# Performance work log

Hardware: AMD Instinct MI355X
Metric: run time of the kernel (lower is better)

Reference implementation:

```python
import jax, jax.numpy as jnp
import numpy as np

EPS = 1e-6
HEADS = 8
DIM_HEAD = 64
SCALE = 16.0
DIM = 1024
INNER = HEADS * DIM_HEAD


def _l2norm(t):
    return t / jnp.clip(jnp.linalg.norm(t, axis=-1, keepdims=True), 1e-12)


def setup_inputs() -> dict:
    key = jax.random.key(0)
    k1, k2, k3, k4 = jax.random.split(key, 4)
    b, n = 2, 4096
    x = jax.random.normal(k1, (b, n, DIM), dtype=jnp.float32)
    # weights stored as [in, out] so application is x @ W
    Wq = jax.random.normal(k2, (DIM, INNER), dtype=jnp.float32) * 0.02
    Wkv = jax.random.normal(k3, (DIM, 2 * INNER), dtype=jnp.float32) * 0.02
    Wo = jax.random.normal(k4, (INNER, DIM), dtype=jnp.float32) * 0.02
    return {"x": x, "Wq": Wq, "Wkv": Wkv, "Wo": Wo}


def reference(x, Wq, Wkv, Wo):
    b, n, _ = x.shape
    q = (x @ Wq).reshape(b, n, HEADS, DIM_HEAD).transpose(0, 2, 1, 3)  # b h n d
    kv = x @ Wkv
    k = kv[..., :INNER].reshape(b, n, HEADS, DIM_HEAD).transpose(0, 2, 1, 3)
    v = kv[..., INNER:].reshape(b, n, HEADS, DIM_HEAD).transpose(0, 2, 1, 3)
    q = _l2norm(q)
    k = _l2norm(k)
    # cosine-sim attention: logits = scale * (q.k) - scale, logits <= 0 so exp is stable
    logits = jnp.einsum('bhid,bhjd->bhij', q, k) * SCALE - SCALE
    p = jnp.exp(logits)
    row_sums = jnp.clip(p.sum(axis=-1, keepdims=True), EPS)  # matches per-block EPS clamp in dense case
    out = jnp.einsum('bhij,bhjd->bhid', p, v) / row_sums  # b h n d
    out = out.transpose(0, 2, 1, 3).reshape(b, n, INNER)
    return out @ Wo
```

## Files before the change

kernel.cpp:

```cpp
#include <hip/hip_runtime.h>


typedef _Float16 f16;
typedef _Float16 f16x4 __attribute__((ext_vector_type(4)));
typedef _Float16 f16x8 __attribute__((ext_vector_type(8)));
typedef float f32x4 __attribute__((ext_vector_type(4)));

#define MFMA_F16(a, b, c) __builtin_amdgcn_mfma_f32_16x16x32_f16((a), (b), (c), 0, 0, 0)

#define QSCALE 23.083120654223414f
#define EXPBIAS -9.083120654223414f

__device__ __forceinline__ void gl_lds16(const void* g, void* l) {
  __builtin_amdgcn_global_load_lds(
      (const __attribute__((address_space(1))) void*)g,
      (__attribute__((address_space(3))) void*)l, 16, 0, 0);
}

__global__ void convert_x_kernel(const float* __restrict__ x, f16* __restrict__ xh, int n8) {
  int i = blockIdx.x * 256 + threadIdx.x;
  if (i >= n8) return;
  const float4* xv = (const float4*)x;
  float4 a = xv[2 * i], b = xv[2 * i + 1];
  f16x8 o;
  o[0] = (f16)a.x; o[1] = (f16)a.y; o[2] = (f16)a.z; o[3] = (f16)a.w;
  o[4] = (f16)b.x; o[5] = (f16)b.y; o[6] = (f16)b.z; o[7] = (f16)b.w;
  ((f16x8*)xh)[i] = o;
}

__global__ void transpose_w_kernel(const float* __restrict__ W, int ldw, int col0,
                                   int K, f16* __restrict__ out) {
  __shared__ float t[64][65];
  int tx = threadIdx.x, ty = threadIdx.y;
  int c0 = blockIdx.x * 64, k0 = blockIdx.y * 64;
#pragma unroll
  for (int i = 0; i < 8; i++)
    t[ty + i * 8][tx] = W[(long)(k0 + ty + i * 8) * ldw + col0 + c0 + tx];
  __syncthreads();
#pragma unroll
  for (int i = 0; i < 8; i++)
    out[(long)(c0 + ty + i * 8) * K + k0 + tx] = (f16)t[tx][ty + i * 8];
}

__global__ void transpose_v_kernel(const f16* __restrict__ Vb, f16* __restrict__ Vt, int n) {
  __shared__ f16 t[64 * 64];
  const int tid = threadIdx.x;
  const int bh = blockIdx.y;
  const int n0 = blockIdx.x * 64;
  const f16* src = Vb + ((long)bh * n + n0) * 64;
  const int j = tid >> 3, c = tid & 7;
  f16x8 v0 = *(const f16x8*)(src + j * 64 + c * 8);
  f16x8 v1 = *(const f16x8*)(src + (j + 32) * 64 + c * 8);
  *(f16x8*)(&t[j * 64 + ((c ^ (j & 7)) << 3)]) = v0;
  *(f16x8*)(&t[(j + 32) * 64 + ((c ^ (j & 7)) << 3)]) = v1;
  __syncthreads();
  const int d = tid >> 3, cj = tid & 7;
  f16x8 o0, o1;
#pragma unroll
  for (int e = 0; e < 8; e++) {
    int jj = cj * 8 + e;
    o0[e] = t[jj * 64 + (((d >> 3) ^ (jj & 7)) << 3) + (d & 7)];
    o1[e] = t[jj * 64 + ((((d + 32) >> 3) ^ (jj & 7)) << 3) + ((d + 32) & 7)];
  }
  *(f16x8*)(Vt + ((long)bh * 64 + d) * n + n0 + cj * 8) = o0;
  *(f16x8*)(Vt + ((long)bh * 64 + d + 32) * n + n0 + cj * 8) = o1;
}

template <int MODE>
__global__ __launch_bounds__(256, 2)
void gemm_kernel(const f16* __restrict__ A, const f16* __restrict__ Bt,
                 float* __restrict__ C,
                 f16* __restrict__ Qb, f16* __restrict__ Kb, f16* __restrict__ Vb,
                 int M, int N, int K) {
  __shared__ f16 As[128 * 32];
  __shared__ f16 Bs[128 * 32];
  const int tid = threadIdx.x;
  const int lane = tid & 63;
  const int wid = tid >> 6;
  const int wr = wid >> 1, wc = wid & 1;
  const int lr = lane & 15, lk = lane >> 4;
  const int lin = blockIdx.x;
  const int bx = ((lin & 7) << 3) | ((lin >> 3) & 7);
  const int by = lin >> 6;
  const long m0 = (long)bx * 128;
  const int n0 = by * 128;

  f32x4 acc[4][4] = {};

  const int c0 = tid, c1 = tid + 256;
  const int ar0 = c0 >> 2, ah0 = (c0 & 3) ^ ((ar0 >> 1) & 3);
  const int ar1 = c1 >> 2, ah1 = (c1 & 3) ^ ((ar1 >> 1) & 3);
  const f16* pa0 = A + (m0 + ar0) * K + ah0 * 8;
  const f16* pa1 = A + (m0 + ar1) * K + ah1 * 8;
  const f16* pb0 = Bt + (long)(n0 + ar0) * K + ah0 * 8;
  const f16* pb1 = Bt + (long)(n0 + ar1) * K + ah1 * 8;

  for (int k0 = 0; k0 < K; k0 += 32) {
    __syncthreads();
    gl_lds16(pa0 + k0, As + c0 * 8);
    gl_lds16(pa1 + k0, As + c1 * 8);
    gl_lds16(pb0 + k0, Bs + c0 * 8);
    gl_lds16(pb1 + k0, Bs + c1 * 8);
    __syncthreads();

    f16x8 af[4], bf[4];
#pragma unroll
    for (int mi = 0; mi < 4; mi++) {
      int row = wr * 64 + mi * 16 + lr;
      int ch = lk ^ ((row >> 1) & 3);
      af[mi] = *(const f16x8*)(As + row * 32 + ch * 8);
    }
#pragma unroll
    for (int ni = 0; ni < 4; ni++) {
      int row = wc * 64 + ni * 16 + lr;
      int ch = lk ^ ((row >> 1) & 3);
      bf[ni] = *(const f16x8*)(Bs + row * 32 + ch * 8);
    }
    __builtin_amdgcn_s_setprio(1);
#pragma unroll
    for (int mi = 0; mi < 4; mi++)
#pragma unroll
      for (int ni = 0; ni < 4; ni++)
        acc[mi][ni] = MFMA_F16(af[mi], bf[ni], acc[mi][ni]);
    __builtin_amdgcn_s_setprio(0);
  }

  if (MODE == 0) {
#pragma unroll
    for (int mi = 0; mi < 4; mi++) {
      long mrow = m0 + wr * 64 + mi * 16 + lk * 4;
#pragma unroll
      for (int r = 0; r < 4; r++)
#pragma unroll
        for (int ni = 0; ni < 4; ni++)
          C[(mrow + r) * N + n0 + wc * 64 + ni * 16 + lr] = acc[mi][ni][r];
    }
  } else {
    const int region = by >> 2;
    const int head = (by & 3) * 2 + wc;
    f16* buf = (region == 0) ? Qb : ((region == 1) ? Kb : Vb);
    const float nscale = (region == 0) ? QSCALE : 1.f;
#pragma unroll
    for (int mi = 0; mi < 4; mi++) {
      float scl[4];
      if (region < 2) {
#pragma unroll
        for (int r = 0; r < 4; r++) {
          float s2 = 0.f;
#pragma unroll
          for (int ni = 0; ni < 4; ni++) s2 += acc[mi][ni][r] * acc[mi][ni][r];
          s2 += __shfl_xor(s2, 1);
          s2 += __shfl_xor(s2, 2);
          s2 += __shfl_xor(s2, 4);
          s2 += __shfl_xor(s2, 8);
          scl[r] = nscale / fmaxf(sqrtf(s2), 1e-12f);
        }
      } else {
#pragma unroll
        for (int r = 0; r < 4; r++) scl[r] = 1.f;
      }
#pragma unroll
      for (int r = 0; r < 4; r++) {
        int m = (int)m0 + wr * 64 + mi * 16 + lk * 4 + r;
        int bb = m >> 12, nn = m & 4095;
        f16* dst = buf + (((long)(bb * 8 + head) * 4096 + nn) << 6);
#pragma unroll
        for (int ni = 0; ni < 4; ni++)
          dst[ni * 16 + lr] = (f16)(acc[mi][ni][r] * scl[r]);
      }
    }
  }
}

__global__ __launch_bounds__(512, 4)
void attn_kernel(const f16* __restrict__ Qb, const f16* __restrict__ Kb,
                 const f16* __restrict__ Vt, f16* __restrict__ Ob, int n) {
  __shared__ f16 Ks[2][128 * 64];
  __shared__ f16 Vs[2][64 * 128];
  __shared__ f16 Ps[8][16 * 64];
  const int tid = threadIdx.x, lane = tid & 63, wid = tid >> 6;
  const int lr = lane & 15, lk = lane >> 4;
  const int lin = blockIdx.x;
  const int bh = (lin & 7) | ((lin >> 8) << 3);
  const int qx = (lin >> 3) & 31;
  const long nl = n;
  const f16* Qg = Qb + (long)bh * nl * 64;
  const f16* Kg = Kb + (long)bh * nl * 64;
  const f16* Vg = Vt + (long)bh * 64 * nl;
  const int q0 = qx * 128 + wid * 16;

  f16x8 qf[2];
#pragma unroll
  for (int kc = 0; kc < 2; kc++)
    qf[kc] = *(const f16x8*)(Qg + (long)(q0 + lr) * 64 + kc * 32 + lk * 8);

  const int krow = tid >> 3;
  const int kcol = ((tid & 7) ^ (krow & 7)) * 8;
  const int vrow = tid >> 4;
  const int vcol = ((tid & 15) ^ (vrow & 15)) * 8;

  f32x4 oacc[4] = {};
  f32x4 osum = {0.f, 0.f, 0.f, 0.f};
  const f32x4 initv = {EXPBIAS, EXPBIAS, EXPBIAS, EXPBIAS};
  f16x8 ones;
#pragma unroll
  for (int e = 0; e < 8; e++) ones[e] = (f16)1.f;

  gl_lds16(Kg + (long)krow * 64 + kcol, &Ks[0][tid * 8]);
  gl_lds16(Kg + (long)(krow + 64) * 64 + kcol, &Ks[0][tid * 8 + 4096]);
  gl_lds16(Vg + (long)vrow * nl + vcol, &Vs[0][tid * 8]);
  gl_lds16(Vg + (long)(vrow + 32) * nl + vcol, &Vs[0][tid * 8 + 4096]);
  __syncthreads();

  const int nt = n >> 7;
  for (int t = 0; t < nt; t++) {
    const int cur = t & 1;
    if (t + 1 < nt) {
      const long j0 = (long)(t + 1) << 7;
      gl_lds16(Kg + (j0 + krow) * 64 + kcol, &Ks[cur ^ 1][tid * 8]);
      gl_lds16(Kg + (j0 + krow + 64) * 64 + kcol, &Ks[cur ^ 1][tid * 8 + 4096]);
      gl_lds16(Vg + (long)vrow * nl + j0 + vcol, &Vs[cur ^ 1][tid * 8]);
      gl_lds16(Vg + (long)(vrow + 32) * nl + j0 + vcol, &Vs[cur ^ 1][tid * 8 + 4096]);
    }

    f32x4 s[8];
    __builtin_amdgcn_s_setprio(1);
#pragma unroll
    for (int jt = 0; jt < 8; jt++) {
      const int j = jt * 16 + lr;
      const f16x8 kf0 = *(const f16x8*)(&Ks[cur][j * 64 + ((lk ^ (j & 7)) << 3)]);
      const f16x8 kf1 = *(const f16x8*)(&Ks[cur][j * 64 + (((4 + lk) ^ (j & 7)) << 3)]);
      f32x4 acc0 = MFMA_F16(kf0, qf[0], initv);
      s[jt] = MFMA_F16(kf1, qf[1], acc0);
    }
    __builtin_amdgcn_s_setprio(0);

#pragma unroll
    for (int sub = 0; sub < 2; sub++) {
#pragma unroll
      for (int jt2 = 0; jt2 < 4; jt2++) {
        const f32x4 sv = s[sub * 4 + jt2];
        const float p0 = __builtin_amdgcn_exp2f(sv[0]);
        const float p1 = __builtin_amdgcn_exp2f(sv[1]);
        const float p2 = __builtin_amdgcn_exp2f(sv[2]);
        const float p3 = __builtin_amdgcn_exp2f(sv[3]);
        const auto h01 = __builtin_amdgcn_cvt_pkrtz(p0, p1);
        const auto h23 = __builtin_amdgcn_cvt_pkrtz(p2, p3);
        f16x4 pk;
        pk[0] = h01[0]; pk[1] = h01[1]; pk[2] = h23[0]; pk[3] = h23[1];
        const int c16 = jt2 * 2 + (lk >> 1);
        *(f16x4*)(&Ps[wid][lr * 64 + ((c16 ^ (lr & 7)) << 3) + ((lk & 1) << 2)]) = pk;
      }

      __builtin_amdgcn_s_setprio(1);
#pragma unroll
      for (int kc2 = 0; kc2 < 2; kc2++) {
        const int c16 = kc2 * 4 + lk;
        const f16x8 pa = *(const f16x8*)(&Ps[wid][lr * 64 + ((c16 ^ (lr & 7)) << 3)]);
        f16x8 vf[4];
#pragma unroll
        for (int dt = 0; dt < 4; dt++) {
          const int d = dt * 16 + lr;
          vf[dt] = *(const f16x8*)(&Vs[cur][d * 128 + (((sub * 8 + kc2 * 4 + lk) ^ (d & 15)) << 3)]);
        }
        osum = MFMA_F16(pa, ones, osum);
#pragma unroll
        for (int dt = 0; dt < 4; dt++)
          oacc[dt] = MFMA_F16(pa, vf[dt], oacc[dt]);
      }
      __builtin_amdgcn_s_setprio(0);
    }

    __syncthreads();
  }

  const int bb = bh >> 3, hh = bh & 7;
#pragma unroll
  for (int r = 0; r < 4; r++) {
    const float inv = 1.f / fmaxf(osum[r], 0.016384f);
    const int qq = q0 + lk * 4 + r;
    f16* dst = Ob + (((long)(bb * 4096 + qq)) << 9) + hh * 64;
#pragma unroll
    for (int dt = 0; dt < 4; dt++)
      dst[dt * 16 + lr] = (f16)(oacc[dt][r] * inv);
  }
}

extern "C" void kernel_launch(void* const* d_in, const int* in_sizes, int n_in,
                              void* d_out, int out_size, void* d_ws, size_t ws_size,
                              hipStream_t stream) {
  const float* x   = (const float*)d_in[0];
  const float* Wq  = (const float*)d_in[1];
  const float* Wkv = (const float*)d_in[2];
  const float* Wo  = (const float*)d_in[3];
  float* out = (float*)d_out;

  char* ws = (char*)d_ws;
  f16* xh     = (f16*)(ws);
  f16* Wqkv_t = (f16*)(ws + 16777216);
  f16* Wo_t   = (f16*)(ws + 19922944);
  f16* Qb     = (f16*)(ws + 20971520);
  f16* Kb     = (f16*)(ws + 29360128);
  f16* Vb     = (f16*)(ws + 37748736);
  f16* At     = (f16*)(ws + 46137344);
  f16* Vt     = xh;

  convert_x_kernel<<<4096, 256, 0, stream>>>(x, xh, 1048576);

  dim3 tb(64, 8);
  transpose_w_kernel<<<dim3(8, 16), tb, 0, stream>>>(Wq, 512, 0, 1024, Wqkv_t);
  transpose_w_kernel<<<dim3(8, 16), tb, 0, stream>>>(Wkv, 1024, 0, 1024, Wqkv_t + 512 * 1024);
  transpose_w_kernel<<<dim3(8, 16), tb, 0, stream>>>(Wkv, 1024, 512, 1024, Wqkv_t + 1024 * 1024);
  transpose_w_kernel<<<dim3(16, 8), tb, 0, stream>>>(Wo, 1024, 0, 512, Wo_t);

  gemm_kernel<1><<<768, 256, 0, stream>>>(xh, Wqkv_t, nullptr, Qb, Kb, Vb,
                                          8192, 1536, 1024);
  transpose_v_kernel<<<dim3(64, 16), 256, 0, stream>>>(Vb, Vt, 4096);
  attn_kernel<<<512, 512, 0, stream>>>(Qb, Kb, Vt, At, 4096);
  gemm_kernel<0><<<512, 256, 0, stream>>>(At, Wo_t, out, nullptr, nullptr, nullptr,
                                          8192, 1024, 512);
}
```

Measured before the change: 163.4 us.

## Use 32x32 MFMA in attention with register P via permlane32 swap

Rewrites the attention kernel to use 32x32x16 MFMA tiles, with 4 waves each handling 32 query rows instead of 8 waves of 16 rows. The exp'd probabilities stay in registers and are reshuffled into the A-operand layout with v_permlane32_swap, which drops the per-wave LDS round trip for P. The row sum is accumulated with fdot2 instead of an extra MFMA against a ones vector. The intent is to cut LDS traffic and MFMA instruction count per FLOP. In exchange it uses fewer threads per block and more accumulator registers, which may lower occupancy and latency hiding.

```diff
diff --git a/kernel.cpp b/kernel.cpp
--- a/kernel.cpp
+++ b/kernel.cpp
@@ -5,8 +5,11 @@
 typedef _Float16 f16x4 __attribute__((ext_vector_type(4)));
 typedef _Float16 f16x8 __attribute__((ext_vector_type(8)));
 typedef float f32x4 __attribute__((ext_vector_type(4)));
+typedef float f32x16 __attribute__((ext_vector_type(16)));
+typedef int i32x4 __attribute__((ext_vector_type(4)));
 
 #define MFMA_F16(a, b, c) __builtin_amdgcn_mfma_f32_16x16x32_f16((a), (b), (c), 0, 0, 0)
+#define MFMA32(a, b, c) __builtin_amdgcn_mfma_f32_32x32x16_f16((a), (b), (c), 0, 0, 0)
 
 #define QSCALE 23.083120654223414f
 #define EXPBIAS -9.083120654223414f
@@ -172,14 +175,13 @@
   }
 }
 
-__global__ __launch_bounds__(512, 4)
+__global__ __launch_bounds__(256, 2)
 void attn_kernel(const f16* __restrict__ Qb, const f16* __restrict__ Kb,
                  const f16* __restrict__ Vt, f16* __restrict__ Ob, int n) {
   __shared__ f16 Ks[2][128 * 64];
   __shared__ f16 Vs[2][64 * 128];
-  __shared__ f16 Ps[8][16 * 64];
   const int tid = threadIdx.x, lane = tid & 63, wid = tid >> 6;
-  const int lr = lane & 15, lk = lane >> 4;
+  const int ql = lane & 31, hi = lane >> 5;
   const int lin = blockIdx.x;
   const int bh = (lin & 7) | ((lin >> 8) << 3);
   const int qx = (lin >> 3) & 31;
@@ -187,102 +189,111 @@
   const f16* Qg = Qb + (long)bh * nl * 64;
   const f16* Kg = Kb + (long)bh * nl * 64;
   const f16* Vg = Vt + (long)bh * 64 * nl;
-  const int q0 = qx * 128 + wid * 16;
-
-  f16x8 qf[2];
-#pragma unroll
-  for (int kc = 0; kc < 2; kc++)
-    qf[kc] = *(const f16x8*)(Qg + (long)(q0 + lr) * 64 + kc * 32 + lk * 8);
-
-  const int krow = tid >> 3;
-  const int kcol = ((tid & 7) ^ (krow & 7)) * 8;
-  const int vrow = tid >> 4;
-  const int vcol = ((tid & 15) ^ (vrow & 15)) * 8;
-
-  f32x4 oacc[4] = {};
-  f32x4 osum = {0.f, 0.f, 0.f, 0.f};
-  const f32x4 initv = {EXPBIAS, EXPBIAS, EXPBIAS, EXPBIAS};
-  f16x8 ones;
-#pragma unroll
-  for (int e = 0; e < 8; e++) ones[e] = (f16)1.f;
-
-  gl_lds16(Kg + (long)krow * 64 + kcol, &Ks[0][tid * 8]);
-  gl_lds16(Kg + (long)(krow + 64) * 64 + kcol, &Ks[0][tid * 8 + 4096]);
-  gl_lds16(Vg + (long)vrow * nl + vcol, &Vs[0][tid * 8]);
-  gl_lds16(Vg + (long)(vrow + 32) * nl + vcol, &Vs[0][tid * 8 + 4096]);
+  const int q0w = qx * 128 + wid * 32;
+
+  f16x8 qf[4];
+#pragma unroll
+  for (int kc = 0; kc < 4; kc++)
+    qf[kc] = *(const f16x8*)(Qg + (long)(q0w + ql) * 64 + kc * 16 + hi * 8);
+
+  int ksrc[4], vsrc[4];
+#pragma unroll
+  for (int p = 0; p < 4; p++) {
+    const int ci = tid + p * 256;
+    const int kj = ci >> 3, kc_ = ci & 7;
+    ksrc[p] = kj * 64 + ((kc_ ^ (kj & 7)) << 3);
+    const int vd = ci >> 4, vc = ci & 15;
+    vsrc[p] = vd * n + ((vc ^ (vd & 15)) << 3);
+  }
+
+  f32x16 oacc[2][2] = {};
+  float rsum = 0.f;
+  f32x16 initv;
+#pragma unroll
+  for (int e = 0; e < 16; e++) initv[e] = EXPBIAS;
+  const auto one2 = __builtin_amdgcn_cvt_pkrtz(1.f, 1.f);
+
+#pragma unroll
+  for (int p = 0; p < 4; p++) {
+    gl_lds16(Kg + ksrc[p], &Ks[0][(tid + p * 256) * 8]);
+    gl_lds16(Vg + vsrc[p], &Vs[0][(tid + p * 256) * 8]);
+  }
   __syncthreads();
 
   const int nt = n >> 7;
   for (int t = 0; t < nt; t++) {
     const int cur = t & 1;
     if (t + 1 < nt) {
-      const long j0 = (long)(t + 1) << 7;
-      gl_lds16(Kg + (j0 + krow) * 64 + kcol, &Ks[cur ^ 1][tid * 8]);
-      gl_lds16(Kg + (j0 + krow + 64) * 64 + kcol, &Ks[cur ^ 1][tid * 8 + 4096]);
-      gl_lds16(Vg + (long)vrow * nl + j0 + vcol, &Vs[cur ^ 1][tid * 8]);
-      gl_lds16(Vg + (long)(vrow + 32) * nl + j0 + vcol, &Vs[cur ^ 1][tid * 8 + 4096]);
-    }
-
-    f32x4 s[8];
+      const long kadv = (long)(t + 1) * 8192;
+      const long vadv = (long)(t + 1) * 128;
+#pragma unroll
+      for (int p = 0; p < 4; p++) {
+        gl_lds16(Kg + kadv + ksrc[p], &Ks[cur ^ 1][(tid + p * 256) * 8]);
+        gl_lds16(Vg + vadv + vsrc[p], &Vs[cur ^ 1][(tid + p * 256) * 8]);
+      }
+    }
+
+    f32x16 s[4];
     __builtin_amdgcn_s_setprio(1);
 #pragma unroll
-    for (int jt = 0; jt < 8; jt++) {
-      const int j = jt * 16 + lr;
-      const f16x8 kf0 = *(const f16x8*)(&Ks[cur][j * 64 + ((lk ^ (j & 7)) << 3)]);
-      const f16x8 kf1 = *(const f16x8*)(&Ks[cur][j * 64 + (((4 + lk) ^ (j & 7)) << 3)]);
-      f32x4 acc0 = MFMA_F16(kf0, qf[0], initv);
-      s[jt] = MFMA_F16(kf1, qf[1], acc0);
+    for (int jt = 0; jt < 4; jt++) {
+      const int j = jt * 32 + ql;
+      const int sw = j & 7;
+      const f16x8 k0 = *(const f16x8*)(&Ks[cur][j * 64 + ((hi ^ sw) << 3)]);
+      s[jt] = MFMA32(k0, qf[0], initv);
+#pragma unroll
+      for (int kc = 1; kc < 4; kc++) {
+        const f16x8 kf = *(const f16x8*)(&Ks[cur][j * 64 + ((((kc << 1) | hi) ^ sw) << 3)]);
+        s[jt] = MFMA32(kf, qf[kc], s[jt]);
+      }
     }
     __builtin_amdgcn_s_setprio(0);
 
 #pragma unroll
-    for (int sub = 0; sub < 2; sub++) {
-#pragma unroll
-      for (int jt2 = 0; jt2 < 4; jt2++) {
-        const f32x4 sv = s[sub * 4 + jt2];
-        const float p0 = __builtin_amdgcn_exp2f(sv[0]);
-        const float p1 = __builtin_amdgcn_exp2f(sv[1]);
-        const float p2 = __builtin_amdgcn_exp2f(sv[2]);
-        const float p3 = __builtin_amdgcn_exp2f(sv[3]);
-        const auto h01 = __builtin_amdgcn_cvt_pkrtz(p0, p1);
-        const auto h23 = __builtin_amdgcn_cvt_pkrtz(p2, p3);
-        f16x4 pk;
-        pk[0] = h01[0]; pk[1] = h01[1]; pk[2] = h23[0]; pk[3] = h23[1];
-        const int c16 = jt2 * 2 + (lk >> 1);
-        *(f16x4*)(&Ps[wid][lr * 64 + ((c16 ^ (lr & 7)) << 3) + ((lk & 1) << 2)]) = pk;
-      }
-
-      __builtin_amdgcn_s_setprio(1);
-#pragma unroll
-      for (int kc2 = 0; kc2 < 2; kc2++) {
-        const int c16 = kc2 * 4 + lk;
-        const f16x8 pa = *(const f16x8*)(&Ps[wid][lr * 64 + ((c16 ^ (lr & 7)) << 3)]);
-        f16x8 vf[4];
-#pragma unroll
-        for (int dt = 0; dt < 4; dt++) {
-          const int d = dt * 16 + lr;
-          vf[dt] = *(const f16x8*)(&Vs[cur][d * 128 + (((sub * 8 + kc2 * 4 + lk) ^ (d & 15)) << 3)]);
+    for (int jt = 0; jt < 4; jt++) {
+      int w[8];
+#pragma unroll
+      for (int m = 0; m < 8; m++) {
+        const float pa = __builtin_amdgcn_exp2f(s[jt][2 * m]);
+        const float pb = __builtin_amdgcn_exp2f(s[jt][2 * m + 1]);
+        const auto h = __builtin_amdgcn_cvt_pkrtz(pa, pb);
+        rsum = __builtin_amdgcn_fdot2(h, one2, rsum, false);
+        w[m] = __builtin_bit_cast(int, h);
+      }
+#pragma unroll
+      for (int kl = 0; kl < 2; kl++) {
+        int a0 = w[4 * kl + 0], a1 = w[4 * kl + 1];
+        int a2 = w[4 * kl + 2], a3 = w[4 * kl + 3];
+        asm volatile("v_permlane32_swap_b32 %0, %1" : "+v"(a0), "+v"(a2));
+        asm volatile("v_permlane32_swap_b32 %0, %1" : "+v"(a1), "+v"(a3));
+        i32x4 fi = {a0, a1, a2, a3};
+        const f16x8 pfrag = __builtin_bit_cast(f16x8, fi);
+        const int kb = jt * 2 + kl;
+        __builtin_amdgcn_s_setprio(1);
+#pragma unroll
+        for (int dt = 0; dt < 2; dt++) {
+          const int d = dt * 32 + ql;
+          const f16x8 vf =
+              *(const f16x8*)(&Vs[cur][d * 128 + ((((kb << 1) | hi) ^ (d & 15)) << 3)]);
+          oacc[kl][dt] = MFMA32(pfrag, vf, oacc[kl][dt]);
         }
-        osum = MFMA_F16(pa, ones, osum);
-#pragma unroll
-        for (int dt = 0; dt < 4; dt++)
-          oacc[dt] = MFMA_F16(pa, vf[dt], oacc[dt]);
-      }
-      __builtin_amdgcn_s_setprio(0);
+        __builtin_amdgcn_s_setprio(0);
+      }
     }
 
     __syncthreads();
   }
 
+  rsum += __shfl_xor(rsum, 32);
   const int bb = bh >> 3, hh = bh & 7;
 #pragma unroll
-  for (int r = 0; r < 4; r++) {
-    const float inv = 1.f / fmaxf(osum[r], 0.016384f);
-    const int qq = q0 + lk * 4 + r;
-    f16* dst = Ob + (((long)(bb * 4096 + qq)) << 9) + hh * 64;
-#pragma unroll
-    for (int dt = 0; dt < 4; dt++)
-      dst[dt * 16 + lr] = (f16)(oacc[dt][r] * inv);
+  for (int r = 0; r < 16; r++) {
+    const int qloc = (r & 3) + 8 * (r >> 2) + 4 * hi;
+    const float sm = __shfl(rsum, qloc);
+    const float inv = 1.f / fmaxf(sm, 0.016384f);
+    f16* dst = Ob + (((long)(bb * 4096 + q0w + qloc)) << 9) + hh * 64;
+    dst[ql] = (f16)((oacc[0][0][r] + oacc[1][0][r]) * inv);
+    dst[32 + ql] = (f16)((oacc[0][1][r] + oacc[1][1][r]) * inv);
   }
 }
 
@@ -316,7 +327,7 @@
   gemm_kernel<1><<<768, 256, 0, stream>>>(xh, Wqkv_t, nullptr, Qb, Kb, Vb,
                                           8192, 1536, 1024);
   transpose_v_kernel<<<dim3(64, 16), 256, 0, stream>>>(Vb, Vt, 4096);
-  attn_kernel<<<512, 512, 0, stream>>>(Qb, Kb, Vt, At, 4096);
+  attn_kernel<<<512, 256, 0, stream>>>(Qb, Kb, Vt, At, 4096);
   gemm_kernel<0><<<512, 256, 0, stream>>>(At, Wo_t, out, nullptr, nullptr, nullptr,
                                           8192, 1024, 512);
 }
```

Result: no change. 162.0 us (-0.9%).
